# Optimization experiments

Measured on AMD Instinct MI355X. Metric: run time of the kernel, lower is better.

The kernel has to match this reference:

```python
import jax, jax.numpy as jnp
import numpy as np

D_MODEL = 2048
DOWN = 512
UP = 1024
NUM_HEADS = 16
ROPE_DIM = 64
BS = 16
SEQ = 512
BASE = 10000.0
HEAD_DIM = D_MODEL // NUM_HEADS          # 128 (used only in the softmax scale)
V_HEAD_DIM = UP // NUM_HEADS             # 64


def _linear(x, W, b):
    # torch nn.Linear: y = x @ W.T + b, W shape (out, in)
    return x @ W.T + b


def _rope(x, num_heads, rope_dim):
    # Faithful to source RotaryEmbedding, including the swapped sin/cos caches:
    #   cos_pos = sin(pos*theta), sin_pos = cos(pos*theta)
    bs, L, _ = x.shape
    q = x.reshape(bs, L, num_heads, rope_dim).transpose(0, 2, 1, 3)  # (bs,h,L,d)
    theta = 1.0 / (BASE ** (jnp.arange(0, rope_dim, 2, dtype=jnp.float32) / rope_dim))
    ang = jnp.arange(L, dtype=jnp.float32)[:, None] * theta[None, :]   # (L, d/2)
    cos_pos = jnp.repeat(jnp.sin(ang), 2, axis=-1)  # (L, d) -- source quirk
    sin_pos = jnp.repeat(jnp.cos(ang), 2, axis=-1)
    q2 = jnp.stack([-q[..., 1::2], q[..., ::2]], axis=-1).reshape(bs, num_heads, L, rope_dim)
    return q * cos_pos + q2 * sin_pos


def setup_inputs() -> dict:
    key = jax.random.key(0)
    ks = jax.random.split(key, 18)
    s = 0.02
    d = {
        "h": jax.random.normal(ks[0], (BS, SEQ, D_MODEL), jnp.float32),
        "W_down_kv": jax.random.normal(ks[1], (DOWN, D_MODEL), jnp.float32) * s,
        "b_down_kv": jnp.zeros((DOWN,), jnp.float32),
        "W_up_k": jax.random.normal(ks[2], (UP, DOWN), jnp.float32) * s,
        "b_up_k": jnp.zeros((UP,), jnp.float32),
        "W_up_v": jax.random.normal(ks[3], (UP, DOWN), jnp.float32) * s,
        "b_up_v": jnp.zeros((UP,), jnp.float32),
        "W_down_q": jax.random.normal(ks[4], (DOWN, D_MODEL), jnp.float32) * s,
        "b_down_q": jnp.zeros((DOWN,), jnp.float32),
        "W_up_q": jax.random.normal(ks[5], (UP, DOWN), jnp.float32) * s,
        "b_up_q": jnp.zeros((UP,), jnp.float32),
        "W_qr": jax.random.normal(ks[6], (ROPE_DIM * NUM_HEADS, DOWN), jnp.float32) * s,
        "b_qr": jnp.zeros((ROPE_DIM * NUM_HEADS,), jnp.float32),
        "W_kr": jax.random.normal(ks[7], (ROPE_DIM, D_MODEL), jnp.float32) * s,
        "b_kr": jnp.zeros((ROPE_DIM,), jnp.float32),
        "W_fc": jax.random.normal(ks[8], (D_MODEL, NUM_HEADS * V_HEAD_DIM), jnp.float32) * s,
        "b_fc": jnp.zeros((D_MODEL,), jnp.float32),
    }
    return d


def reference(h, W_down_kv, b_down_kv, W_up_k, b_up_k, W_up_v, b_up_v,
              W_down_q, b_down_q, W_up_q, b_up_q, W_qr, b_qr,
              W_kr, b_kr, W_fc, b_fc):
    bs, L, _ = h.shape
    # low-rank KV path
    c_kv = _linear(h, W_down_kv, b_down_kv)             # (bs,L,down)
    k_c = _linear(c_kv, W_up_k, b_up_k)                 # (bs,L,up)
    v_c = _linear(c_kv, W_up_v, b_up_v)                 # (bs,L,up)
    # low-rank Q path
    c_q = _linear(h, W_down_q, b_down_q)                # (bs,L,down)
    q_c = _linear(c_q, W_up_q, b_up_q)                  # (bs,L,up)
    # rope (decoupled) path
    q_r = _rope(_linear(c_q, W_qr, b_qr), NUM_HEADS, ROPE_DIM)  # (bs,H,L,rope)
    k_r = _rope(_linear(h, W_kr, b_kr), 1, ROPE_DIM)            # (bs,1,L,rope)

    q_c = q_c.reshape(bs, L, NUM_HEADS, -1).transpose(0, 2, 1, 3)  # (bs,H,L,64)
    q = jnp.concatenate([q_c, q_r], axis=-1)                        # (bs,H,L,128)
    k_c = k_c.reshape(bs, L, NUM_HEADS, -1).transpose(0, 2, 1, 3)
    k_r = jnp.broadcast_to(k_r, (bs, NUM_HEADS, L, ROPE_DIM))       # shared across heads
    k = jnp.concatenate([k_c, k_r], axis=-1)

    scale = 1.0 / jnp.sqrt(jnp.float32(HEAD_DIM + ROPE_DIM))  # sqrt(192), per source
    scores = jnp.einsum('bhqd,bhkd->bhqk', q, k) * scale
    attn = jax.nn.softmax(scores, axis=-1)  # dropout is identity in eval mode

    v = v_c.reshape(bs, L, NUM_HEADS, V_HEAD_DIM).transpose(0, 2, 1, 3)
    out = jnp.einsum('bhqk,bhkd->bhqd', attn, v)
    out = out.transpose(0, 2, 1, 3).reshape(bs, L, -1)   # (bs,L,H*v_head_dim)
    return _linear(out, W_fc, b_fc)                      # (bs,L,d_model)
```

## Files before the change

kernel.cpp:

```cpp
#include <hip/hip_runtime.h>
#include <hip/hip_bf16.h>

typedef __bf16 bf16x8 __attribute__((ext_vector_type(8)));
typedef float f32x4 __attribute__((ext_vector_type(4)));
using u16 = unsigned short;
using u32 = unsigned int;

__device__ __forceinline__ float bf2f(u16 v) {
    unsigned int u = (unsigned int)v << 16;
    float f; __builtin_memcpy(&f, &u, 4); return f;
}
__device__ __forceinline__ u16 f2bf(float f) {
    unsigned int u; __builtin_memcpy(&u, &f, 4);
    u += 0x7FFFu + ((u >> 16) & 1u);
    return (u16)(u >> 16);
}

struct Cvt9 {
    const float* src[9];
    u16* dst[9];
    int end[9];
};
__global__ __launch_bounds__(256) void cvt_all(Cvt9 d, int total)
{
    int c = blockIdx.x * 256 + threadIdx.x;
    if (c >= total) return;
    int seg = 0;
    while (c >= d.end[seg]) ++seg;
    int local = c - (seg ? d.end[seg - 1] : 0);
    const float* s = d.src[seg] + (size_t)local * 8;
    float4 f0 = *(const float4*)s;
    float4 f1 = *(const float4*)(s + 4);
    u16 tmp[8] = { f2bf(f0.x), f2bf(f0.y), f2bf(f0.z), f2bf(f0.w),
                   f2bf(f1.x), f2bf(f1.y), f2bf(f1.z), f2bf(f1.w) };
    *(uint4*)(d.dst[seg] + (size_t)local * 8) = *(const uint4*)tmp;
}

struct Cpy7 {
    const float* src[7];
    float* dst[7];
    int end[7];
};
__global__ __launch_bounds__(256) void copy_f32(Cpy7 d, int total)
{
    int c = blockIdx.x * 256 + threadIdx.x;
    if (c >= total) return;
    int seg = 0;
    while (c >= d.end[seg]) ++seg;
    int local = c - (seg ? d.end[seg - 1] : 0);
    d.dst[seg][local] = d.src[seg][local];
}

template<bool CF>
__global__ __launch_bounds__(256) void gemm_v3(
    const u16* __restrict__ A0, const u16* __restrict__ B0, void* __restrict__ C0, const float* __restrict__ e0,
    const u16* __restrict__ A1, const u16* __restrict__ B1, void* __restrict__ C1, const float* __restrict__ e1,
    int ysplit, int lda, int ldb, int ldc, int N, int K)
{
    __shared__ __align__(16) u16 As[128 * 32];
    __shared__ __align__(16) u16 Bs[128 * 32];

    const int t = threadIdx.x;
    const int lane = t & 63;
    const int w = t >> 6;
    const int wm = w >> 1, wn = w & 1;
    const int l16 = lane & 15, quad = lane >> 4;
    const int m0 = blockIdx.x * 128;

    const u16* A; const u16* B; void* Cv; const float* bias; int yl;
    if ((int)blockIdx.y < ysplit) { A = A0; B = B0; Cv = C0; bias = e0; yl = blockIdx.y; }
    else                          { A = A1; B = B1; Cv = C1; bias = e1; yl = blockIdx.y - ysplit; }
    const int n0 = yl * 128;

    const int sub  = lane >> 2;
    const int slot = lane & 3;
    const int agc  = slot ^ ((sub >> 1) & 3);
    const int sfr  = (l16 >> 1) & 3;

    f32x4 acc[4][4];
#pragma unroll
    for (int i = 0; i < 4; ++i)
#pragma unroll
        for (int j = 0; j < 4; ++j) acc[i][j] = (f32x4){0.f, 0.f, 0.f, 0.f};

    for (int k0 = 0; k0 < K; k0 += 32) {
        __syncthreads();
#pragma unroll
        for (int c = 0; c < 2; ++c) {
            const int rr = w * 32 + c * 16;
            const u16* ga = A + (size_t)(m0 + rr + sub) * lda + k0 + agc * 8;
            __builtin_amdgcn_global_load_lds(
                (const __attribute__((address_space(1))) u32*)ga,
                (__attribute__((address_space(3))) u32*)&As[rr * 32], 16, 0, 0);
            const u16* gb = B + (size_t)(n0 + rr + sub) * ldb + k0 + agc * 8;
            __builtin_amdgcn_global_load_lds(
                (const __attribute__((address_space(1))) u32*)gb,
                (__attribute__((address_space(3))) u32*)&Bs[rr * 32], 16, 0, 0);
        }
        __syncthreads();

        bf16x8 af[4], bfr[4];
#pragma unroll
        for (int i = 0; i < 4; ++i)
            af[i] = *(const bf16x8*)&As[(wm * 64 + i * 16 + l16) * 32 + (quad ^ sfr) * 8];
#pragma unroll
        for (int j = 0; j < 4; ++j)
            bfr[j] = *(const bf16x8*)&Bs[(wn * 64 + j * 16 + l16) * 32 + (quad ^ sfr) * 8];
#pragma unroll
        for (int i = 0; i < 4; ++i)
#pragma unroll
            for (int j = 0; j < 4; ++j)
                acc[i][j] = __builtin_amdgcn_mfma_f32_16x16x32_bf16(af[i], bfr[j], acc[i][j], 0, 0, 0);
    }

#pragma unroll
    for (int j = 0; j < 4; ++j) {
        int col = n0 + wn * 64 + j * 16 + l16;
        if (col >= N) continue;
        float bv = bias[col];
#pragma unroll
        for (int i = 0; i < 4; ++i) {
#pragma unroll
            for (int r = 0; r < 4; ++r) {
                int row = m0 + wm * 64 + i * 16 + quad * 4 + r;
                float v = acc[i][j][r] + bv;
                if (CF) ((float*)Cv)[(size_t)row * ldc + col] = v;
                else    ((u16*)Cv)[(size_t)row * ldc + col] = f2bf(v);
            }
        }
    }
}

__global__ void rope_inplace(u16* __restrict__ buf, int ld, int col0, int ppr, int total)
{
    int idx = blockIdx.x * 256 + threadIdx.x;
    if (idx >= total) return;
    int row = idx / ppr;
    int pi  = idx - row * ppr;
    int grp = pi >> 5;
    int i   = pi & 31;
    int pos = row & 511;
    float theta = __expf(-(float)i * 0.2878231366242558f);
    float ang = (float)pos * theta;
    float s = sinf(ang), c = cosf(ang);
    size_t base = (size_t)row * ld + col0 + grp * 64 + 2 * i;
    float x0 = bf2f(buf[base]);
    float x1 = bf2f(buf[base + 1]);
    buf[base]     = f2bf(x0 * s - x1 * c);
    buf[base + 1] = f2bf(x1 * s + x0 * c);
}

__global__ __launch_bounds__(256) void attn_kernel(
    const u16* __restrict__ q_src,
    const u16* __restrict__ kv_src,
    const u16* __restrict__ kr_src,
    u16* __restrict__ o_dst, int ldo)
{
    __shared__ __align__(16) u16 Ks[64 * 136];
    __shared__ __align__(16) u16 Vt[64 * 72];
    __shared__ __align__(16) u16 Ps[64 * 72];

    const int t = threadIdx.x;
    const int lane = t & 63;
    const int w = t >> 6;
    const int l16 = lane & 15, quad = lane >> 4;
    const int qt = blockIdx.x;
    const int h  = blockIdx.y;
    const int b  = blockIdx.z;
    const int qrow0 = b * 512 + qt * 64;

    bf16x8 aq[4];
    {
        const u16* qrow = q_src + (size_t)(qrow0 + w * 16 + l16) * 2048;
#pragma unroll
        for (int ks = 0; ks < 4; ++ks) {
            int col = ks * 32 + quad * 8;
            const u16* src = (col < 64) ? qrow + h * 64 + col
                                        : qrow + 1024 + h * 64 + (col - 64);
            aq[ks] = *(const bf16x8*)src;
        }
    }

    float m_run[4], l_run[4];
    f32x4 o[4];
#pragma unroll
    for (int r = 0; r < 4; ++r) { m_run[r] = -1e30f; l_run[r] = 0.f; }
#pragma unroll
    for (int n = 0; n < 4; ++n) o[n] = (f32x4){0.f, 0.f, 0.f, 0.f};

    const float scale = 0.07216878364870323f;
    const int Rp = (64 - (quad << 4)) & 48;
    const int Rr = (64 - ((l16 >> 2) << 4)) & 48;

    for (int kt = 0; kt < 8; ++kt) {
        __syncthreads();
        const int krow0 = b * 512 + kt * 64;
#pragma unroll
        for (int p = 0; p < 4; ++p) {
            int ch = t + 256 * p;
            int r = ch >> 4;
            int col = (ch & 15) * 8;
            const u16* src = (col < 64)
                ? kv_src + (size_t)(krow0 + r) * 2048 + h * 64 + col
                : kr_src + (size_t)(krow0 + r) * 1088 + 1024 + (col - 64);
            *(uint4*)&Ks[r * 136 + col] = *(const uint4*)src;
        }
#pragma unroll
        for (int p = 0; p < 2; ++p) {
            int ch = t + 256 * p;
            int r = ch >> 3;
            int v0 = (ch & 7) * 8;
            uint4 vv = *(const uint4*)(kv_src + (size_t)(krow0 + r) * 2048 + 1024 + h * 64 + v0);
            u16 tmp[8];
            __builtin_memcpy(tmp, &vv, 16);
            int rot = (r + v0) & 63;
#pragma unroll
            for (int j2 = 0; j2 < 8; ++j2)
                Vt[(v0 + j2) * 72 + rot] = tmp[j2];
        }
        __syncthreads();

        f32x4 s[4];
#pragma unroll
        for (int n = 0; n < 4; ++n) s[n] = (f32x4){0.f, 0.f, 0.f, 0.f};
#pragma unroll
        for (int ks = 0; ks < 4; ++ks) {
#pragma unroll
            for (int n = 0; n < 4; ++n) {
                bf16x8 bk = *(const bf16x8*)&Ks[(n * 16 + l16) * 136 + ks * 32 + quad * 8];
                s[n] = __builtin_amdgcn_mfma_f32_16x16x32_bf16(aq[ks], bk, s[n], 0, 0, 0);
            }
        }

        float mx[4], alpha[4], rs[4];
#pragma unroll
        for (int r = 0; r < 4; ++r) {
#pragma unroll
            for (int n = 0; n < 4; ++n) s[n][r] *= scale;
            mx[r] = fmaxf(fmaxf(s[0][r], s[1][r]), fmaxf(s[2][r], s[3][r]));
        }
#pragma unroll
        for (int d = 1; d < 16; d <<= 1)
#pragma unroll
            for (int r = 0; r < 4; ++r)
                mx[r] = fmaxf(mx[r], __shfl_xor(mx[r], d));
#pragma unroll
        for (int r = 0; r < 4; ++r) {
            float mnew = fmaxf(m_run[r], mx[r]);
            alpha[r] = __expf(m_run[r] - mnew);
            m_run[r] = mnew;
            rs[r] = 0.f;
#pragma unroll
            for (int n = 0; n < 4; ++n) {
                float pv = __expf(s[n][r] - mnew);
                s[n][r] = pv;
                rs[r] += pv;
            }
        }
#pragma unroll
        for (int d = 1; d < 16; d <<= 1)
#pragma unroll
            for (int r = 0; r < 4; ++r)
                rs[r] += __shfl_xor(rs[r], d);
#pragma unroll
        for (int r = 0; r < 4; ++r) {
            l_run[r] = l_run[r] * alpha[r] + rs[r];
#pragma unroll
            for (int n = 0; n < 4; ++n) o[n][r] *= alpha[r];
        }

#pragma unroll
        for (int n = 0; n < 4; ++n) {
            int pc = (n * 16 + l16 + Rp) & 63;
#pragma unroll
            for (int r = 0; r < 4; ++r)
                Ps[(w * 16 + quad * 4 + r) * 72 + pc] = f2bf(s[n][r]);
        }

#pragma unroll
        for (int kk = 0; kk < 2; ++kk) {
            bf16x8 ap = *(const bf16x8*)&Ps[(w * 16 + l16) * 72 + ((kk * 32 + quad * 8 + Rr) & 63)];
#pragma unroll
            for (int n = 0; n < 4; ++n) {
                bf16x8 bv = *(const bf16x8*)&Vt[(n * 16 + l16) * 72
                              + ((kk * 32 + quad * 8 + n * 16 + (l16 & 8)) & 63)];
                o[n] = __builtin_amdgcn_mfma_f32_16x16x32_bf16(ap, bv, o[n], 0, 0, 0);
            }
        }
    }

#pragma unroll
    for (int n = 0; n < 4; ++n) {
#pragma unroll
        for (int r = 0; r < 4; ++r) {
            int row = qrow0 + w * 16 + quad * 4 + r;
            int col = h * 64 + n * 16 + l16;
            o_dst[(size_t)row * ldo + col] = f2bf(o[n][r] / l_run[r]);
        }
    }
}

extern "C" void kernel_launch(void* const* d_in, const int* in_sizes, int n_in,
                              void* d_out, int out_size, void* d_ws, size_t ws_size,
                              hipStream_t stream)
{
    const float* h    = (const float*)d_in[0];
    const float* Wdkv = (const float*)d_in[1];
    const float* bdkv = (const float*)d_in[2];
    const float* Wuk  = (const float*)d_in[3];
    const float* buk  = (const float*)d_in[4];
    const float* Wuv  = (const float*)d_in[5];
    const float* buv  = (const float*)d_in[6];
    const float* Wdq  = (const float*)d_in[7];
    const float* bdq  = (const float*)d_in[8];
    const float* Wuq  = (const float*)d_in[9];
    const float* buq  = (const float*)d_in[10];
    const float* Wqr  = (const float*)d_in[11];
    const float* bqr  = (const float*)d_in[12];
    const float* Wkr  = (const float*)d_in[13];
    const float* bkr  = (const float*)d_in[14];
    const float* Wfc  = (const float*)d_in[15];
    const float* bfc  = (const float*)d_in[16];

    char* ws = (char*)d_ws;
    u16* out1   = (u16*)ws;
    u16* hbf    = (u16*)(ws + 17825792);
    u16* out2a  = hbf;
    u16* out2b  = (u16*)(ws + 51380224);
    u16* w1     = (u16*)(ws + 84934656);
    u16* w2a    = (u16*)(ws + 89653248);
    u16* w2b    = (u16*)(ws + 91750400);
    u16* wfc    = (u16*)(ws + 93847552);
    float* bias_s1 = (float*)(ws + 98041856);
    float* bias_2  = (float*)(ws + 98046208);

    Cvt9 cd;
    const float* srcs[9] = { h, Wdkv, Wdq, Wkr, Wuk, Wuv, Wuq, Wqr, Wfc };
    u16* dsts[9] = { hbf, w1, w1 + 512 * 2048, w1 + 1024 * 2048,
                     w2a, w2a + 1024 * 512, w2b, w2b + 1024 * 512, wfc };
    int cnts[9] = { 2097152, 131072, 131072, 16384, 65536, 65536, 65536, 65536, 262144 };
    int acc2 = 0;
    for (int i = 0; i < 9; ++i) { cd.src[i] = srcs[i]; cd.dst[i] = dsts[i]; acc2 += cnts[i]; cd.end[i] = acc2; }
    cvt_all<<<(acc2 + 255) / 256, 256, 0, stream>>>(cd, acc2);
    hipMemsetAsync(w1 + 1088 * 2048, 0, 64 * 2048 * sizeof(u16), stream);

    Cpy7 bc;
    const float* bs[7] = { bdkv, bdq, bkr, buk, buv, buq, bqr };
    float* bd[7] = { bias_s1, bias_s1 + 512, bias_s1 + 1024,
                     bias_2, bias_2 + 1024, bias_2 + 2048, bias_2 + 3072 };
    int bn[7] = { 512, 512, 64, 1024, 1024, 1024, 1024 };
    int bacc = 0;
    for (int i = 0; i < 7; ++i) { bc.src[i] = bs[i]; bc.dst[i] = bd[i]; bacc += bn[i]; bc.end[i] = bacc; }
    copy_f32<<<(bacc + 255) / 256, 256, 0, stream>>>(bc, bacc);

    gemm_v3<false><<<dim3(64, 9), 256, 0, stream>>>(
        hbf, w1, out1, bias_s1,
        hbf, w1, out1, bias_s1, 9, 2048, 2048, 1088, 1088, 2048);
    rope_inplace<<<1024, 256, 0, stream>>>(out1, 1088, 1024, 32, 8192 * 32);

    gemm_v3<false><<<dim3(64, 32), 256, 0, stream>>>(
        out1,       w2a, out2a, bias_2,
        out1 + 512, w2b, out2b, bias_2 + 2048, 16, 1088, 512, 2048, 2048, 512);
    rope_inplace<<<16384, 256, 0, stream>>>(out2b, 2048, 1024, 512, 8192 * 512);

    attn_kernel<<<dim3(8, 16, 16), 256, 0, stream>>>(out2b, out2a, out1, out1, 1088);

    gemm_v3<true><<<dim3(64, 16), 256, 0, stream>>>(
        out1, wfc, d_out, bfc,
        out1, wfc, d_out, bfc, 16, 1088, 1024, 2048, 2048, 1024);
}
```

Measured before the change: 454.2 us.

## Deepen GEMM K tile, prefetch attention K/V tiles, use exp2 softmax

The GEMM K-step grows from 32 to 64 with a new XOR swizzle over 64-column rows, which halves the number of barrier-separated load phases. The attention kernel now register-double-buffers the next K/V tile so the global loads overlap the current tile's compute. It also folds the scale and log2(e) into a single exp2 FMA, uses a reciprocal multiply in the epilogue, and reorders the grid so heads vary fastest. The cost is more LDS per GEMM block and more registers in attention, which may lower occupancy.

```diff
diff --git a/kernel.cpp b/kernel.cpp
--- a/kernel.cpp
+++ b/kernel.cpp
@@ -57,8 +57,8 @@
     const u16* __restrict__ A1, const u16* __restrict__ B1, void* __restrict__ C1, const float* __restrict__ e1,
     int ysplit, int lda, int ldb, int ldc, int N, int K)
 {
-    __shared__ __align__(16) u16 As[128 * 32];
-    __shared__ __align__(16) u16 Bs[128 * 32];
+    __shared__ __align__(16) u16 As[128 * 64];
+    __shared__ __align__(16) u16 Bs[128 * 64];
 
     const int t = threadIdx.x;
     const int lane = t & 63;
@@ -72,10 +72,8 @@
     else                          { A = A1; B = B1; Cv = C1; bias = e1; yl = blockIdx.y - ysplit; }
     const int n0 = yl * 128;
 
-    const int sub  = lane >> 2;
-    const int slot = lane & 3;
-    const int agc  = slot ^ ((sub >> 1) & 3);
-    const int sfr  = (l16 >> 1) & 3;
+    const int rowi = lane >> 3;
+    const int gc   = (lane & 7) ^ rowi;
 
     f32x4 acc[4][4];
 #pragma unroll
@@ -83,34 +81,38 @@
 #pragma unroll
         for (int j = 0; j < 4; ++j) acc[i][j] = (f32x4){0.f, 0.f, 0.f, 0.f};
 
-    for (int k0 = 0; k0 < K; k0 += 32) {
+    for (int k0 = 0; k0 < K; k0 += 64) {
         __syncthreads();
 #pragma unroll
-        for (int c = 0; c < 2; ++c) {
-            const int rr = w * 32 + c * 16;
-            const u16* ga = A + (size_t)(m0 + rr + sub) * lda + k0 + agc * 8;
+        for (int i = 0; i < 4; ++i) {
+            const int rr = w * 32 + i * 8;
+            const u16* ga = A + (size_t)(m0 + rr + rowi) * lda + k0 + gc * 8;
             __builtin_amdgcn_global_load_lds(
                 (const __attribute__((address_space(1))) u32*)ga,
-                (__attribute__((address_space(3))) u32*)&As[rr * 32], 16, 0, 0);
-            const u16* gb = B + (size_t)(n0 + rr + sub) * ldb + k0 + agc * 8;
+                (__attribute__((address_space(3))) u32*)&As[rr * 64], 16, 0, 0);
+            const u16* gb = B + (size_t)(n0 + rr + rowi) * ldb + k0 + gc * 8;
             __builtin_amdgcn_global_load_lds(
                 (const __attribute__((address_space(1))) u32*)gb,
-                (__attribute__((address_space(3))) u32*)&Bs[rr * 32], 16, 0, 0);
+                (__attribute__((address_space(3))) u32*)&Bs[rr * 64], 16, 0, 0);
         }
         __syncthreads();
 
-        bf16x8 af[4], bfr[4];
-#pragma unroll
-        for (int i = 0; i < 4; ++i)
-            af[i] = *(const bf16x8*)&As[(wm * 64 + i * 16 + l16) * 32 + (quad ^ sfr) * 8];
-#pragma unroll
-        for (int j = 0; j < 4; ++j)
-            bfr[j] = *(const bf16x8*)&Bs[(wn * 64 + j * 16 + l16) * 32 + (quad ^ sfr) * 8];
-#pragma unroll
-        for (int i = 0; i < 4; ++i)
+#pragma unroll
+        for (int kk = 0; kk < 2; ++kk) {
+            const int cc = (((kk << 2) + quad) ^ (l16 & 7)) << 3;
+            bf16x8 af[4], bfr[4];
+#pragma unroll
+            for (int i = 0; i < 4; ++i)
+                af[i] = *(const bf16x8*)&As[(wm * 64 + i * 16 + l16) * 64 + cc];
 #pragma unroll
             for (int j = 0; j < 4; ++j)
-                acc[i][j] = __builtin_amdgcn_mfma_f32_16x16x32_bf16(af[i], bfr[j], acc[i][j], 0, 0, 0);
+                bfr[j] = *(const bf16x8*)&Bs[(wn * 64 + j * 16 + l16) * 64 + cc];
+#pragma unroll
+            for (int i = 0; i < 4; ++i)
+#pragma unroll
+                for (int j = 0; j < 4; ++j)
+                    acc[i][j] = __builtin_amdgcn_mfma_f32_16x16x32_bf16(af[i], bfr[j], acc[i][j], 0, 0, 0);
+        }
     }
 
 #pragma unroll
@@ -164,10 +166,11 @@
     const int lane = t & 63;
     const int w = t >> 6;
     const int l16 = lane & 15, quad = lane >> 4;
-    const int qt = blockIdx.x;
-    const int h  = blockIdx.y;
-    const int b  = blockIdx.z;
+    const int h  = blockIdx.x;
+    const int b  = blockIdx.y;
+    const int qt = blockIdx.z;
     const int qrow0 = b * 512 + qt * 64;
+    const int krow_base = b * 512;
 
     bf16x8 aq[4];
     {
@@ -181,42 +184,66 @@
         }
     }
 
-    float m_run[4], l_run[4];
+    const int colK = (t & 15) * 8;
+    const int r0k  = t >> 4;
+    const u16* kbase; int kstr;
+    if (colK < 64) { kbase = kv_src + h * 64 + colK;        kstr = 2048; }
+    else           { kbase = kr_src + 1024 + (colK - 64);   kstr = 1088; }
+    u16* kw = &Ks[r0k * 136 + colK];
+
+    const int v00 = (t & 7) * 8;
+    const int r0v = t >> 3;
+    const u16* vbase = kv_src + 1024 + h * 64 + v00;
+    const int rotA = (r0v + v00) & 63;
+    const int rotB = (r0v + 32 + v00) & 63;
+    u16* vwA = &Vt[v00 * 72 + rotA];
+    u16* vwB = &Vt[v00 * 72 + rotB];
+
+    auto LOADT = [&](int krow0, uint4& K0, uint4& K1, uint4& K2, uint4& K3,
+                     uint4& V0, uint4& V1) {
+        K0 = *(const uint4*)(kbase + (size_t)(krow0 + r0k     ) * kstr);
+        K1 = *(const uint4*)(kbase + (size_t)(krow0 + r0k + 16) * kstr);
+        K2 = *(const uint4*)(kbase + (size_t)(krow0 + r0k + 32) * kstr);
+        K3 = *(const uint4*)(kbase + (size_t)(krow0 + r0k + 48) * kstr);
+        V0 = *(const uint4*)(vbase + (size_t)(krow0 + r0v     ) * 2048);
+        V1 = *(const uint4*)(vbase + (size_t)(krow0 + r0v + 32) * 2048);
+    };
+    auto WRITET = [&](const uint4& K0, const uint4& K1, const uint4& K2, const uint4& K3,
+                      const uint4& V0, const uint4& V1) {
+        *(uint4*)(kw)            = K0;
+        *(uint4*)(kw + 16 * 136) = K1;
+        *(uint4*)(kw + 32 * 136) = K2;
+        *(uint4*)(kw + 48 * 136) = K3;
+        u16 ta[8], tb[8];
+        __builtin_memcpy(ta, &V0, 16);
+        __builtin_memcpy(tb, &V1, 16);
+#pragma unroll
+        for (int j2 = 0; j2 < 8; ++j2) { vwA[j2 * 72] = ta[j2]; vwB[j2 * 72] = tb[j2]; }
+    };
+
+    float m2[4], l_run[4];
     f32x4 o[4];
 #pragma unroll
-    for (int r = 0; r < 4; ++r) { m_run[r] = -1e30f; l_run[r] = 0.f; }
+    for (int r = 0; r < 4; ++r) { m2[r] = -1e30f; l_run[r] = 0.f; }
 #pragma unroll
     for (int n = 0; n < 4; ++n) o[n] = (f32x4){0.f, 0.f, 0.f, 0.f};
 
-    const float scale = 0.07216878364870323f;
+    const float C = 0.10411756f;
     const int Rp = (64 - (quad << 4)) & 48;
     const int Rr = (64 - ((l16 >> 2) << 4)) & 48;
 
+    uint4 kA0, kA1, kA2, kA3, vA0, vA1;
+    uint4 kB0, kB1, kB2, kB3, vB0, vB1;
+    LOADT(krow_base, kA0, kA1, kA2, kA3, vA0, vA1);
+
     for (int kt = 0; kt < 8; ++kt) {
         __syncthreads();
-        const int krow0 = b * 512 + kt * 64;
-#pragma unroll
-        for (int p = 0; p < 4; ++p) {
-            int ch = t + 256 * p;
-            int r = ch >> 4;
-            int col = (ch & 15) * 8;
-            const u16* src = (col < 64)
-                ? kv_src + (size_t)(krow0 + r) * 2048 + h * 64 + col
-                : kr_src + (size_t)(krow0 + r) * 1088 + 1024 + (col - 64);
-            *(uint4*)&Ks[r * 136 + col] = *(const uint4*)src;
-        }
-#pragma unroll
-        for (int p = 0; p < 2; ++p) {
-            int ch = t + 256 * p;
-            int r = ch >> 3;
-            int v0 = (ch & 7) * 8;
-            uint4 vv = *(const uint4*)(kv_src + (size_t)(krow0 + r) * 2048 + 1024 + h * 64 + v0);
-            u16 tmp[8];
-            __builtin_memcpy(tmp, &vv, 16);
-            int rot = (r + v0) & 63;
-#pragma unroll
-            for (int j2 = 0; j2 < 8; ++j2)
-                Vt[(v0 + j2) * 72 + rot] = tmp[j2];
+        if ((kt & 1) == 0) {
+            WRITET(kA0, kA1, kA2, kA3, vA0, vA1);
+            if (kt < 7) LOADT(krow_base + (kt + 1) * 64, kB0, kB1, kB2, kB3, vB0, vB1);
+        } else {
+            WRITET(kB0, kB1, kB2, kB3, vB0, vB1);
+            if (kt < 7) LOADT(krow_base + (kt + 1) * 64, kA0, kA1, kA2, kA3, vA0, vA1);
         }
         __syncthreads();
 
@@ -234,11 +261,8 @@
 
         float mx[4], alpha[4], rs[4];
 #pragma unroll
-        for (int r = 0; r < 4; ++r) {
-#pragma unroll
-            for (int n = 0; n < 4; ++n) s[n][r] *= scale;
+        for (int r = 0; r < 4; ++r)
             mx[r] = fmaxf(fmaxf(s[0][r], s[1][r]), fmaxf(s[2][r], s[3][r]));
-        }
 #pragma unroll
         for (int d = 1; d < 16; d <<= 1)
 #pragma unroll
@@ -246,13 +270,13 @@
                 mx[r] = fmaxf(mx[r], __shfl_xor(mx[r], d));
 #pragma unroll
         for (int r = 0; r < 4; ++r) {
-            float mnew = fmaxf(m_run[r], mx[r]);
-            alpha[r] = __expf(m_run[r] - mnew);
-            m_run[r] = mnew;
+            float mnew = fmaxf(m2[r], mx[r] * C);
+            alpha[r] = __builtin_amdgcn_exp2f(m2[r] - mnew);
+            m2[r] = mnew;
             rs[r] = 0.f;
 #pragma unroll
             for (int n = 0; n < 4; ++n) {
-                float pv = __expf(s[n][r] - mnew);
+                float pv = __builtin_amdgcn_exp2f(__builtin_fmaf(s[n][r], C, -mnew));
                 s[n][r] = pv;
                 rs[r] += pv;
             }
@@ -290,12 +314,13 @@
     }
 
 #pragma unroll
-    for (int n = 0; n < 4; ++n) {
-#pragma unroll
-        for (int r = 0; r < 4; ++r) {
-            int row = qrow0 + w * 16 + quad * 4 + r;
+    for (int r = 0; r < 4; ++r) {
+        float inv = 1.0f / l_run[r];
+        int row = qrow0 + w * 16 + quad * 4 + r;
+#pragma unroll
+        for (int n = 0; n < 4; ++n) {
             int col = h * 64 + n * 16 + l16;
-            o_dst[(size_t)row * ldo + col] = f2bf(o[n][r] / l_run[r]);
+            o_dst[(size_t)row * ldo + col] = f2bf(o[n][r] * inv);
         }
     }
 }
@@ -363,7 +388,7 @@
         out1 + 512, w2b, out2b, bias_2 + 2048, 16, 1088, 512, 2048, 2048, 512);
     rope_inplace<<<16384, 256, 0, stream>>>(out2b, 2048, 1024, 512, 8192 * 512);
 
-    attn_kernel<<<dim3(8, 16, 16), 256, 0, stream>>>(out2b, out2a, out1, out1, 1088);
+    attn_kernel<<<dim3(16, 16, 8), 256, 0, stream>>>(out2b, out2a, out1, out1, 1088);
 
     gemm_v3<true><<<dim3(64, 16), 256, 0, stream>>>(
         out1, wfc, d_out, bfc,
```

New measurement: 448.0 us. About the same (-1.4%).
